# Optimization experiments

Measured on AMD Instinct MI355X. Metric: run time of the kernel, lower is better.

Reference implementation:

```python
import jax, jax.numpy as jnp
import numpy as np
from jax import lax

B, L = 128, 26          # batch, sequence length (25-iteration loop => L = 26)
C1, C2 = 128, 64        # conv channel widths (n_filters)
K1, K2 = 7, 5           # conv kernel sizes
N_POS = 25              # hardcoded position loop in original module
H = 1 + L * C2 + (C2 * C2) * (N_POS * (N_POS + 1) // 2)  # 1332865


def setup_inputs() -> dict:
    key = jax.random.key(0)
    ks = jax.random.split(key, 6)
    x = jax.random.randint(ks[0], (B, L), 0, 4)                      # nucleotide ids 0..3
    conv1_w = jax.random.normal(ks[1], (C1, 4, K1), jnp.float32) * 0.1
    conv1_b = jnp.zeros((C1,), jnp.float32)
    conv2_w = jax.random.normal(ks[2], (C2, C1, K2), jnp.float32) * 0.05
    conv2_b = jnp.zeros((C2,), jnp.float32)
    reg_w = jax.random.normal(ks[3], (1, H), jnp.float32) * 0.001
    reg_b = jnp.zeros((1,), jnp.float32)
    return {"x": x, "conv1_w": conv1_w, "conv1_b": conv1_b,
            "conv2_w": conv2_w, "conv2_b": conv2_b,
            "reg_w": reg_w, "reg_b": reg_b}


def _conv1d_same_relu(h, w, b):
    # torch Conv1d(padding=k//2) + ReLU; dropout p=0.0 is identity (eval)
    k = w.shape[-1]
    y = lax.conv_general_dilated(h, w, (1,), [(k // 2, k // 2)],
                                 dimension_numbers=('NCH', 'OIH', 'NCH'))
    return jax.nn.relu(y + b[None, :, None])


def reference(x, conv1_w, conv1_b, conv2_w, conv2_b, reg_w, reg_b):
    # one_hot(x).transpose(1,2) -> [B, 4, L]
    h = jax.nn.one_hot(x, 4, dtype=jnp.float32).transpose(0, 2, 1)
    h = _conv1d_same_relu(h, conv1_w, conv1_b)   # [B, C1, L]
    h = _conv1d_same_relu(h, conv2_w, conv2_b)   # [B, C2, L]
    # permute(0,2,1).reshape(B, -1): position-major, channel-minor flat features
    feat = h.transpose(0, 2, 1).reshape(h.shape[0], -1)  # [B, L*C2]
    # pairwise quadratic expansion: for position i, channel j -> feat[:, i*C+j] * feat[:, (i+1)*C:]
    # vectorized per-position as an outer product; 25-iteration structural loop only
    parts = []
    for i in range(N_POS):
        a = feat[:, i * C2:(i + 1) * C2]          # [B, C2]
        b = feat[:, (i + 1) * C2:]                # [B, (L-1-i)*C2]
        parts.append((a[:, :, None] * b[:, None, :]).reshape(feat.shape[0], -1))
    x_second_order = jnp.concatenate(parts, axis=1)       # [B, 325*C2^2]
    full = jnp.concatenate(
        [jnp.ones((feat.shape[0], 1), jnp.float32), feat, x_second_order], axis=1)  # [B, H]
    out = full @ reg_w[0] + reg_b[0]              # Linear(H, 1) -> squeeze -> [B]
    return out
```

## Files before the change

kernel.cpp:

```cpp
#include <hip/hip_runtime.h>

#define B_   128
#define L_   26
#define C1_  128
#define C2_  64
#define K1_  7
#define K2_  5
#define NPOS 25
#define FEAT (L_*C2_)
#define NPAIR (NPOS*(NPOS+1)/2)

#define HROW 132
#define WROW 644

__global__ __launch_bounds__(256) void conv_kernel(
    const int*   __restrict__ x,
    const float* __restrict__ w1, const float* __restrict__ b1,
    const float* __restrict__ w2, const float* __restrict__ b2,
    float* __restrict__ featT)
{
    __shared__ float h1s[30*HROW];
    __shared__ float w2s[16*WROW];
    __shared__ float w1s[4*K1_*C1_];
    __shared__ int   xs[L_];

    const int bid = blockIdx.x;
    const int b   = bid >> 2;
    const int c2t = bid & 3;
    const int t   = threadIdx.x;

    if (t < L_) xs[t] = x[b*L_ + t];
    if (t < HROW) { h1s[0*HROW+t] = 0.f; h1s[1*HROW+t] = 0.f;
                    h1s[28*HROW+t] = 0.f; h1s[29*HROW+t] = 0.f; }

    for (int i = t; i < C1_*4*K1_; i += 256) {
        const int c1  = i / (4*K1_);
        const int rem = i - c1*(4*K1_);
        const int nt  = rem / K1_;
        const int k   = rem - nt*K1_;
        w1s[(nt*K1_ + k)*C1_ + c1] = w1[i];
    }

    {
        const float* src = w2 + c2t*16*C1_*K2_;
        for (int idx = t; idx < 16*C1_*K2_; idx += 256) {
            const int c2i = idx / (C1_*K2_);
            const int rem = idx - c2i*(C1_*K2_);
            const int c1  = rem / K2_;
            const int k   = rem - c1*K2_;
            w2s[c2i*WROW + k*C1_ + c1] = src[idx];
        }
    }
    __syncthreads();

    for (int idx = t; idx < C1_*L_; idx += 256) {
        const int c1 = idx & 127;
        const int l  = idx >> 7;
        float s = b1[c1];
        #pragma unroll
        for (int k = 0; k < K1_; ++k) {
            const int pos = l + k - 3;
            if (pos >= 0 && pos < L_)
                s += w1s[(xs[pos]*K1_ + k)*C1_ + c1];
        }
        h1s[(l+2)*HROW + c1] = fmaxf(s, 0.f);
    }
    __syncthreads();

    if (t < 16*13) {
        const int c2i = t & 15;
        const int lg  = t >> 4;
        const int l0  = 2*lg, l1 = 2*lg + 1;
        float a0 = 0.f, a1 = 0.f, a2 = 0.f, a3 = 0.f;
        #pragma unroll
        for (int k = 0; k < K2_; ++k) {
            const float4* wrow = (const float4*)&w2s[c2i*WROW + k*C1_];
            const float4* h0r  = (const float4*)&h1s[(l0 + k)*HROW];
            const float4* h1r  = (const float4*)&h1s[(l1 + k)*HROW];
            #pragma unroll
            for (int cq = 0; cq < 32; cq += 2) {
                const float4 w0 = wrow[cq],  w1v = wrow[cq+1];
                const float4 x0 = h0r[cq],   x1 = h0r[cq+1];
                const float4 y0 = h1r[cq],   y1 = h1r[cq+1];
                a0 += w0.x*x0.x + w0.y*x0.y + w0.z*x0.z + w0.w*x0.w;
                a1 += w1v.x*x1.x + w1v.y*x1.y + w1v.z*x1.z + w1v.w*x1.w;
                a2 += w0.x*y0.x + w0.y*y0.y + w0.z*y0.z + w0.w*y0.w;
                a3 += w1v.x*y1.x + w1v.y*y1.y + w1v.z*y1.z + w1v.w*y1.w;
            }
        }
        const int   c2  = c2t*16 + c2i;
        const float bb  = b2[c2];
        featT[(l0*C2_ + c2)*B_ + b] = fmaxf(a0 + a1 + bb, 0.f);
        featT[(l1*C2_ + c2)*B_ + b] = fmaxf(a2 + a3 + bb, 0.f);
    }
}

__global__ __launch_bounds__(256) void reg_kernel(
    const float* __restrict__ featT,
    const float* __restrict__ rw, const float* __restrict__ rb,
    float* __restrict__ part)
{
    __shared__ float ws[64*64];
    __shared__ float red0[256], red1[256];
    const int t  = threadIdx.x;
    const int b0 = t & 63;
    const int wv = t >> 6;
    const int bid = blockIdx.x;

    float acc0 = 0.f, acc1 = 0.f;

    if (bid == NPAIR) {
        const int u0 = wv * (FEAT/4);
        for (int u = u0; u < u0 + FEAT/4; ++u) {
            const float w = rw[1 + u];
            acc0 += featT[u*B_ + b0]      * w;
            acc1 += featT[u*B_ + b0 + 64] * w;
        }
        if (wv == 0) { const float c = rw[0] + rb[0]; acc0 += c; acc1 += c; }
    } else {
        int i = 0, r = bid;
        while (r >= NPOS - i) { r -= NPOS - i; ++i; }
        const int j = i + 1 + r;

        const int stride = (NPOS - i) * 64;
        const int base   = 1 + FEAT + 4096*(NPOS*i - (i*(i-1))/2)
                         + (j - i - 1)*64;

        #pragma unroll
        for (int k = 0; k < 16; ++k) {
            const int idx = t + k*256;
            ws[idx] = rw[base + (idx >> 6)*stride + (idx & 63)];
        }
        __syncthreads();

        const int p0 = wv * 16;
        float sp0[16], sp1[16];
        #pragma unroll
        for (int pp = 0; pp < 16; ++pp) { sp0[pp] = 0.f; sp1[pp] = 0.f; }

        const float* fj = &featT[j*64*B_ + b0];
        #pragma unroll 4
        for (int g = 0; g < 16; ++g) {
            const float f00 = fj[(g*4+0)*B_],      f01 = fj[(g*4+1)*B_],
                        f02 = fj[(g*4+2)*B_],      f03 = fj[(g*4+3)*B_];
            const float f10 = fj[(g*4+0)*B_ + 64], f11 = fj[(g*4+1)*B_ + 64],
                        f12 = fj[(g*4+2)*B_ + 64], f13 = fj[(g*4+3)*B_ + 64];
            #pragma unroll
            for (int pp = 0; pp < 16; ++pp) {
                const float4 w = *(const float4*)&ws[(p0 + pp)*64 + g*4];
                sp0[pp] += w.x*f00 + w.y*f01 + w.z*f02 + w.w*f03;
                sp1[pp] += w.x*f10 + w.y*f11 + w.z*f12 + w.w*f13;
            }
        }

        const float* fi = &featT[(i*64 + p0)*B_ + b0];
        #pragma unroll
        for (int pp = 0; pp < 16; ++pp) {
            acc0 += fi[pp*B_]      * sp0[pp];
            acc1 += fi[pp*B_ + 64] * sp1[pp];
        }
    }

    red0[t] = acc0;
    red1[t] = acc1;
    __syncthreads();
    if (t < B_) {
        const int bb = t & 63;
        const float* rr = (t < 64) ? red0 : red1;
        part[bid*B_ + t] = (rr[bb] + rr[64+bb]) + (rr[128+bb] + rr[192+bb]);
    }
}

__global__ __launch_bounds__(128) void fin_kernel(
    const float* __restrict__ part, float* __restrict__ out)
{
    const int b = threadIdx.x;
    float s0 = 0.f, s1 = 0.f, s2 = 0.f, s3 = 0.f;
    int p = 0;
    for (; p + 4 <= NPAIR + 1; p += 4) {
        s0 += part[(p+0)*B_ + b];
        s1 += part[(p+1)*B_ + b];
        s2 += part[(p+2)*B_ + b];
        s3 += part[(p+3)*B_ + b];
    }
    for (; p < NPAIR + 1; ++p) s0 += part[p*B_ + b];
    out[b] = (s0 + s1) + (s2 + s3);
}

extern "C" void kernel_launch(void* const* d_in, const int* in_sizes, int n_in,
                              void* d_out, int out_size, void* d_ws, size_t ws_size,
                              hipStream_t stream)
{
    const int*   x  = (const int*)  d_in[0];
    const float* w1 = (const float*)d_in[1];
    const float* b1 = (const float*)d_in[2];
    const float* w2 = (const float*)d_in[3];
    const float* b2 = (const float*)d_in[4];
    const float* rw = (const float*)d_in[5];
    const float* rb = (const float*)d_in[6];
    float* out   = (float*)d_out;
    float* featT = (float*)d_ws;
    float* part  = (float*)((char*)d_ws + 851968);

    conv_kernel<<<dim3(512), dim3(256), 0, stream>>>(x, w1, b1, w2, b2, featT);
    reg_kernel <<<dim3(NPAIR+1), dim3(256), 0, stream>>>(featT, rw, rb, part);
    fin_kernel <<<dim3(1), dim3(128), 0, stream>>>(part, out);
}
```

Before: 115.0 us.

## Fuse final reduction into reg kernel via last-block counter; rebalance conv tiling

The separate final-sum kernel is removed. Each reg block now bumps an atomic counter after writing its partial, and the last block to arrive sums all partials into the output, which saves one kernel launch. The conv kernel now runs 256 blocks of 128 threads, each covering half the output channels. Each thread computes 4 channels × 2 positions so weight and activation loads from shared memory are reused more. The conv kernel resets the counter to zero each call, which relies on stream ordering, and conv has fewer, larger blocks that use more shared memory each.

New measurement: 141.3 us. 1.23x slower.

```diff
diff --git a/kernel.cpp b/kernel.cpp
--- a/kernel.cpp
+++ b/kernel.cpp
@@ -11,29 +11,33 @@
 #define NPAIR (NPOS*(NPOS+1)/2)
 
 #define HROW 132
-#define WROW 644
-
-__global__ __launch_bounds__(256) void conv_kernel(
+#define W2ROW 644
+
+__global__ __launch_bounds__(128) void conv_kernel(
     const int*   __restrict__ x,
     const float* __restrict__ w1, const float* __restrict__ b1,
     const float* __restrict__ w2, const float* __restrict__ b2,
-    float* __restrict__ featT)
+    float* __restrict__ featT, int* __restrict__ counter)
 {
+    __shared__ float w2s[32*W2ROW];
     __shared__ float h1s[30*HROW];
-    __shared__ float w2s[16*WROW];
     __shared__ float w1s[4*K1_*C1_];
     __shared__ int   xs[L_];
 
-    const int bid = blockIdx.x;
-    const int b   = bid >> 2;
-    const int c2t = bid & 3;
-    const int t   = threadIdx.x;
+    const int bid  = blockIdx.x;
+    const int b    = bid >> 1;
+    const int half = bid & 1;
+    const int t    = threadIdx.x;
+
+    if (bid == 0 && t == 0) *counter = 0;
 
     if (t < L_) xs[t] = x[b*L_ + t];
-    if (t < HROW) { h1s[0*HROW+t] = 0.f; h1s[1*HROW+t] = 0.f;
-                    h1s[28*HROW+t] = 0.f; h1s[29*HROW+t] = 0.f; }
-
-    for (int i = t; i < C1_*4*K1_; i += 256) {
+    for (int i = t; i < HROW; i += 128) {
+        h1s[0*HROW+i] = 0.f; h1s[1*HROW+i] = 0.f;
+        h1s[28*HROW+i] = 0.f; h1s[29*HROW+i] = 0.f;
+    }
+
+    for (int i = t; i < C1_*4*K1_; i += 128) {
         const int c1  = i / (4*K1_);
         const int rem = i - c1*(4*K1_);
         const int nt  = rem / K1_;
@@ -42,18 +46,21 @@
     }
 
     {
-        const float* src = w2 + c2t*16*C1_*K2_;
-        for (int idx = t; idx < 16*C1_*K2_; idx += 256) {
-            const int c2i = idx / (C1_*K2_);
-            const int rem = idx - c2i*(C1_*K2_);
-            const int c1  = rem / K2_;
-            const int k   = rem - c1*K2_;
-            w2s[c2i*WROW + k*C1_ + c1] = src[idx];
-        }
-    }
-    __syncthreads();
-
-    for (int idx = t; idx < C1_*L_; idx += 256) {
+        const float* src = w2 + half*32*C1_*K2_;
+        #pragma unroll
+        for (int i = 0; i < 32; ++i) {
+            const int p  = t + i*128;
+            const int c2 = p >> 7;
+            const int c1 = p & 127;
+            const float* s5 = src + p*5;
+            float* dst = &w2s[c2*W2ROW + c1];
+            dst[0*C1_] = s5[0]; dst[1*C1_] = s5[1]; dst[2*C1_] = s5[2];
+            dst[3*C1_] = s5[3]; dst[4*C1_] = s5[4];
+        }
+    }
+    __syncthreads();
+
+    for (int idx = t; idx < C1_*L_; idx += 128) {
         const int c1 = idx & 127;
         const int l  = idx >> 7;
         float s = b1[c1];
@@ -67,41 +74,63 @@
     }
     __syncthreads();
 
-    if (t < 16*13) {
-        const int c2i = t & 15;
-        const int lg  = t >> 4;
-        const int l0  = 2*lg, l1 = 2*lg + 1;
-        float a0 = 0.f, a1 = 0.f, a2 = 0.f, a3 = 0.f;
-        #pragma unroll
+    if (t < 104) {
+        const int c2t = t / 13;
+        const int lt  = t - c2t*13;
+        const int l0  = 2*lt, l1 = l0 + 1;
+
+        float acc00=0.f, acc01=0.f, acc02=0.f, acc03=0.f;
+        float acc10=0.f, acc11=0.f, acc12=0.f, acc13=0.f;
+        const float* wbase = &w2s[(c2t*4)*W2ROW];
+
         for (int k = 0; k < K2_; ++k) {
-            const float4* wrow = (const float4*)&w2s[c2i*WROW + k*C1_];
-            const float4* h0r  = (const float4*)&h1s[(l0 + k)*HROW];
-            const float4* h1r  = (const float4*)&h1s[(l1 + k)*HROW];
-            #pragma unroll
-            for (int cq = 0; cq < 32; cq += 2) {
-                const float4 w0 = wrow[cq],  w1v = wrow[cq+1];
-                const float4 x0 = h0r[cq],   x1 = h0r[cq+1];
-                const float4 y0 = h1r[cq],   y1 = h1r[cq+1];
-                a0 += w0.x*x0.x + w0.y*x0.y + w0.z*x0.z + w0.w*x0.w;
-                a1 += w1v.x*x1.x + w1v.y*x1.y + w1v.z*x1.z + w1v.w*x1.w;
-                a2 += w0.x*y0.x + w0.y*y0.y + w0.z*y0.z + w0.w*y0.w;
-                a3 += w1v.x*y1.x + w1v.y*y1.y + w1v.z*y1.z + w1v.w*y1.w;
+            const float4* hr0 = (const float4*)&h1s[(l0 + k)*HROW];
+            const float4* hr1 = (const float4*)&h1s[(l1 + k)*HROW];
+            const float*  wk  = wbase + k*C1_;
+            #pragma unroll 4
+            for (int q = 0; q < 32; ++q) {
+                const float4 h0 = hr0[q];
+                const float4 h1v = hr1[q];
+                const float4 w0 = *(const float4*)&wk[0*W2ROW + q*4];
+                const float4 w1v= *(const float4*)&wk[1*W2ROW + q*4];
+                const float4 w2v= *(const float4*)&wk[2*W2ROW + q*4];
+                const float4 w3 = *(const float4*)&wk[3*W2ROW + q*4];
+                acc00 += w0.x*h0.x + w0.y*h0.y + w0.z*h0.z + w0.w*h0.w;
+                acc01 += w1v.x*h0.x + w1v.y*h0.y + w1v.z*h0.z + w1v.w*h0.w;
+                acc02 += w2v.x*h0.x + w2v.y*h0.y + w2v.z*h0.z + w2v.w*h0.w;
+                acc03 += w3.x*h0.x + w3.y*h0.y + w3.z*h0.z + w3.w*h0.w;
+                acc10 += w0.x*h1v.x + w0.y*h1v.y + w0.z*h1v.z + w0.w*h1v.w;
+                acc11 += w1v.x*h1v.x + w1v.y*h1v.y + w1v.z*h1v.z + w1v.w*h1v.w;
+                acc12 += w2v.x*h1v.x + w2v.y*h1v.y + w2v.z*h1v.z + w2v.w*h1v.w;
+                acc13 += w3.x*h1v.x + w3.y*h1v.y + w3.z*h1v.z + w3.w*h1v.w;
             }
         }
-        const int   c2  = c2t*16 + c2i;
-        const float bb  = b2[c2];
-        featT[(l0*C2_ + c2)*B_ + b] = fmaxf(a0 + a1 + bb, 0.f);
-        featT[(l1*C2_ + c2)*B_ + b] = fmaxf(a2 + a3 + bb, 0.f);
+
+        const int c2g = half*32 + c2t*4;
+        const float bb0 = b2[c2g+0], bb1 = b2[c2g+1],
+                    bb2 = b2[c2g+2], bb3 = b2[c2g+3];
+        float* f0 = &featT[(l0*C2_ + c2g)*B_ + b];
+        float* f1 = &featT[(l1*C2_ + c2g)*B_ + b];
+        f0[0*B_] = fmaxf(acc00 + bb0, 0.f);
+        f0[1*B_] = fmaxf(acc01 + bb1, 0.f);
+        f0[2*B_] = fmaxf(acc02 + bb2, 0.f);
+        f0[3*B_] = fmaxf(acc03 + bb3, 0.f);
+        f1[0*B_] = fmaxf(acc10 + bb0, 0.f);
+        f1[1*B_] = fmaxf(acc11 + bb1, 0.f);
+        f1[2*B_] = fmaxf(acc12 + bb2, 0.f);
+        f1[3*B_] = fmaxf(acc13 + bb3, 0.f);
     }
 }
 
 __global__ __launch_bounds__(256) void reg_kernel(
     const float* __restrict__ featT,
     const float* __restrict__ rw, const float* __restrict__ rb,
-    float* __restrict__ part)
+    float* __restrict__ part, int* __restrict__ counter,
+    float* __restrict__ out)
 {
     __shared__ float ws[64*64];
     __shared__ float red0[256], red1[256];
+    __shared__ int   isLast;
     const int t  = threadIdx.x;
     const int b0 = t & 63;
     const int wv = t >> 6;
@@ -169,22 +198,26 @@
         const float* rr = (t < 64) ? red0 : red1;
         part[bid*B_ + t] = (rr[bb] + rr[64+bb]) + (rr[128+bb] + rr[192+bb]);
     }
-}
-
-__global__ __launch_bounds__(128) void fin_kernel(
-    const float* __restrict__ part, float* __restrict__ out)
-{
-    const int b = threadIdx.x;
-    float s0 = 0.f, s1 = 0.f, s2 = 0.f, s3 = 0.f;
-    int p = 0;
-    for (; p + 4 <= NPAIR + 1; p += 4) {
-        s0 += part[(p+0)*B_ + b];
-        s1 += part[(p+1)*B_ + b];
-        s2 += part[(p+2)*B_ + b];
-        s3 += part[(p+3)*B_ + b];
-    }
-    for (; p < NPAIR + 1; ++p) s0 += part[p*B_ + b];
-    out[b] = (s0 + s1) + (s2 + s3);
+
+    __threadfence();
+    __syncthreads();
+    if (t == 0) isLast = (atomicAdd(counter, 1) == NPAIR);
+    __syncthreads();
+    if (isLast) {
+        __threadfence();
+        if (t < B_) {
+            float s0 = 0.f, s1 = 0.f, s2 = 0.f, s3 = 0.f;
+            int p = 0;
+            for (; p + 4 <= NPAIR + 1; p += 4) {
+                s0 += part[(p+0)*B_ + t];
+                s1 += part[(p+1)*B_ + t];
+                s2 += part[(p+2)*B_ + t];
+                s3 += part[(p+3)*B_ + t];
+            }
+            for (; p < NPAIR + 1; ++p) s0 += part[p*B_ + t];
+            out[t] = (s0 + s1) + (s2 + s3);
+        }
+    }
 }
 
 extern "C" void kernel_launch(void* const* d_in, const int* in_sizes, int n_in,
@@ -198,11 +231,13 @@
     const float* b2 = (const float*)d_in[4];
     const float* rw = (const float*)d_in[5];
     const float* rb = (const float*)d_in[6];
-    float* out   = (float*)d_out;
-    float* featT = (float*)d_ws;
-    float* part  = (float*)((char*)d_ws + 851968);
-
-    conv_kernel<<<dim3(512), dim3(256), 0, stream>>>(x, w1, b1, w2, b2, featT);
-    reg_kernel <<<dim3(NPAIR+1), dim3(256), 0, stream>>>(featT, rw, rb, part);
-    fin_kernel <<<dim3(1), dim3(128), 0, stream>>>(part, out);
+    float* out     = (float*)d_out;
+    float* featT   = (float*)d_ws;
+    float* part    = (float*)((char*)d_ws + 851968);
+    int*   counter = (int*)  ((char*)d_ws + 851968 + 166912);
+
+    conv_kernel<<<dim3(256), dim3(128), 0, stream>>>(x, w1, b1, w2, b2,
+                                                     featT, counter);
+    reg_kernel <<<dim3(NPAIR+1), dim3(256), 0, stream>>>(featT, rw, rb,
+                                                         part, counter, out);
 }
```

## Split conv stage into separate conv1 and conv2 kernels with batch-minor layout

Applied to the files above, without the earlier changes.

The fused per-sample conv kernel is replaced by two kernels. The first computes conv1 with threads mapped to batch and writes a zero-padded, batch-minor h1 buffer to global memory. The second computes conv2 per (position, 8-channel group), splitting the C1 reduction across four waves and combining the partial sums in shared memory. This is meant to cut the redundant per-block reloading of w2 and the low thread utilisation of the old kernel, at the cost of an extra launch and a global round-trip for h1.

Result: slower. 126.9 us (+10.3%).

```diff
diff --git a/kernel.cpp b/kernel.cpp
--- a/kernel.cpp
+++ b/kernel.cpp
@@ -9,89 +9,121 @@
 #define NPOS 25
 #define FEAT (L_*C2_)
 #define NPAIR (NPOS*(NPOS+1)/2)
-
-#define HROW 132
-#define WROW 644
-
-__global__ __launch_bounds__(256) void conv_kernel(
+#define HR   30
+
+
+__global__ __launch_bounds__(128) void s_kernel(
     const int*   __restrict__ x,
     const float* __restrict__ w1, const float* __restrict__ b1,
-    const float* __restrict__ w2, const float* __restrict__ b2,
-    float* __restrict__ featT)
-{
-    __shared__ float h1s[30*HROW];
-    __shared__ float w2s[16*WROW];
-    __shared__ float w1s[4*K1_*C1_];
-    __shared__ int   xs[L_];
-
+    float* __restrict__ h1g)
+{
     const int bid = blockIdx.x;
-    const int b   = bid >> 2;
-    const int c2t = bid & 3;
     const int t   = threadIdx.x;
 
-    if (t < L_) xs[t] = x[b*L_ + t];
-    if (t < HROW) { h1s[0*HROW+t] = 0.f; h1s[1*HROW+t] = 0.f;
-                    h1s[28*HROW+t] = 0.f; h1s[29*HROW+t] = 0.f; }
-
-    for (int i = t; i < C1_*4*K1_; i += 256) {
-        const int c1  = i / (4*K1_);
-        const int rem = i - c1*(4*K1_);
-        const int nt  = rem / K1_;
-        const int k   = rem - nt*K1_;
-        w1s[(nt*K1_ + k)*C1_ + c1] = w1[i];
-    }
-
-    {
-        const float* src = w2 + c2t*16*C1_*K2_;
-        for (int idx = t; idx < 16*C1_*K2_; idx += 256) {
-            const int c2i = idx / (C1_*K2_);
-            const int rem = idx - c2i*(C1_*K2_);
-            const int c1  = rem / K2_;
-            const int k   = rem - c1*K2_;
-            w2s[c2i*WROW + k*C1_ + c1] = src[idx];
-        }
-    }
-    __syncthreads();
-
-    for (int idx = t; idx < C1_*L_; idx += 256) {
-        const int c1 = idx & 127;
-        const int l  = idx >> 7;
-        float s = b1[c1];
+    if (bid >= 104) {
+        const int z   = bid - 104;
+        const int c1q = z >> 2;
+        const int pr  = z & 3;
+        const int row = (pr < 2) ? pr : 26 + pr;
+        #pragma unroll
+        for (int ci = 0; ci < 32; ++ci)
+            h1g[((c1q*32 + ci)*HR + row)*B_ + t] = 0.f;
+        return;
+    }
+
+    const int l   = bid % 26;
+    const int c1q = bid / 26;
+
+    __shared__ float w1s[4*K1_*32];
+    for (int i = t; i < 4*K1_*32; i += 128) {
+        const int ci  = i / (4*K1_);
+        const int rem = i - ci*(4*K1_);
+        w1s[rem*32 + ci] = w1[(c1q*32 + ci)*(4*K1_) + rem];
+    }
+    __syncthreads();
+
+    int xv[K1_];
+    #pragma unroll
+    for (int k = 0; k < K1_; ++k) {
+        const int pos = l + k - 3;
+        xv[k] = (pos >= 0 && pos < L_) ? x[t*L_ + pos] : 0;
+    }
+
+    for (int ci = 0; ci < 32; ++ci) {
+        float s = b1[c1q*32 + ci];
         #pragma unroll
         for (int k = 0; k < K1_; ++k) {
             const int pos = l + k - 3;
             if (pos >= 0 && pos < L_)
-                s += w1s[(xs[pos]*K1_ + k)*C1_ + c1];
-        }
-        h1s[(l+2)*HROW + c1] = fmaxf(s, 0.f);
-    }
-    __syncthreads();
-
-    if (t < 16*13) {
-        const int c2i = t & 15;
-        const int lg  = t >> 4;
-        const int l0  = 2*lg, l1 = 2*lg + 1;
-        float a0 = 0.f, a1 = 0.f, a2 = 0.f, a3 = 0.f;
+                s += w1s[(xv[k]*K1_ + k)*32 + ci];
+        }
+        h1g[((c1q*32 + ci)*HR + (l + 2))*B_ + t] = fmaxf(s, 0.f);
+    }
+}
+
+__global__ __launch_bounds__(256) void g_kernel(
+    const float* __restrict__ h1g,
+    const float* __restrict__ w2, const float* __restrict__ b2,
+    float* __restrict__ featT)
+{
+    __shared__ float w2s[K2_*C1_*8];
+    __shared__ float red[4*8*B_];
+
+    const int bid = blockIdx.x;
+    const int l   = bid % 26;
+    const int c2o = bid / 26;
+    const int t   = threadIdx.x;
+    const int wv  = t >> 6;
+    const int b0  = t & 63;
+
+    for (int idx = t; idx < K2_*C1_*8; idx += 256) {
+        const int c2i = idx / (C1_*K2_);
+        const int rem = idx - c2i*(C1_*K2_);
+        const int c1  = rem / K2_;
+        const int k   = rem - c1*K2_;
+        w2s[(k*C1_ + c1)*8 + c2i] = w2[(c2o*8 + c2i)*(C1_*K2_) + rem];
+    }
+    __syncthreads();
+
+    float acc[8][2];
+    #pragma unroll
+    for (int c = 0; c < 8; ++c) { acc[c][0] = 0.f; acc[c][1] = 0.f; }
+
+    const int cb = wv*32;
+    for (int c1i = 0; c1i < 32; ++c1i) {
+        const int c1 = cb + c1i;
+        const float* hbase = &h1g[(c1*HR + l)*B_];
         #pragma unroll
         for (int k = 0; k < K2_; ++k) {
-            const float4* wrow = (const float4*)&w2s[c2i*WROW + k*C1_];
-            const float4* h0r  = (const float4*)&h1s[(l0 + k)*HROW];
-            const float4* h1r  = (const float4*)&h1s[(l1 + k)*HROW];
-            #pragma unroll
-            for (int cq = 0; cq < 32; cq += 2) {
-                const float4 w0 = wrow[cq],  w1v = wrow[cq+1];
-                const float4 x0 = h0r[cq],   x1 = h0r[cq+1];
-                const float4 y0 = h1r[cq],   y1 = h1r[cq+1];
-                a0 += w0.x*x0.x + w0.y*x0.y + w0.z*x0.z + w0.w*x0.w;
-                a1 += w1v.x*x1.x + w1v.y*x1.y + w1v.z*x1.z + w1v.w*x1.w;
-                a2 += w0.x*y0.x + w0.y*y0.y + w0.z*y0.z + w0.w*y0.w;
-                a3 += w1v.x*y1.x + w1v.y*y1.y + w1v.z*y1.z + w1v.w*y1.w;
-            }
-        }
-        const int   c2  = c2t*16 + c2i;
-        const float bb  = b2[c2];
-        featT[(l0*C2_ + c2)*B_ + b] = fmaxf(a0 + a1 + bb, 0.f);
-        featT[(l1*C2_ + c2)*B_ + b] = fmaxf(a2 + a3 + bb, 0.f);
+            const float h0 = hbase[k*B_ + b0];
+            const float h1 = hbase[k*B_ + b0 + 64];
+            const float4* wp = (const float4*)&w2s[(k*C1_ + c1)*8];
+            const float4 wa = wp[0], wb = wp[1];
+            acc[0][0] += wa.x*h0;  acc[0][1] += wa.x*h1;
+            acc[1][0] += wa.y*h0;  acc[1][1] += wa.y*h1;
+            acc[2][0] += wa.z*h0;  acc[2][1] += wa.z*h1;
+            acc[3][0] += wa.w*h0;  acc[3][1] += wa.w*h1;
+            acc[4][0] += wb.x*h0;  acc[4][1] += wb.x*h1;
+            acc[5][0] += wb.y*h0;  acc[5][1] += wb.y*h1;
+            acc[6][0] += wb.z*h0;  acc[6][1] += wb.z*h1;
+            acc[7][0] += wb.w*h0;  acc[7][1] += wb.w*h1;
+        }
+    }
+
+    #pragma unroll
+    for (int c = 0; c < 8; ++c) {
+        red[(wv*8 + c)*B_ + b0]      = acc[c][0];
+        red[(wv*8 + c)*B_ + b0 + 64] = acc[c][1];
+    }
+    __syncthreads();
+
+    for (int u = t; u < 8*B_; u += 256) {
+        const int c2i = u >> 7;
+        const int bb  = u & 127;
+        float s = red[(0*8 + c2i)*B_ + bb] + red[(1*8 + c2i)*B_ + bb]
+                + red[(2*8 + c2i)*B_ + bb] + red[(3*8 + c2i)*B_ + bb];
+        s += b2[c2o*8 + c2i];
+        featT[(l*C2_ + c2o*8 + c2i)*B_ + bb] = fmaxf(s, 0.f);
     }
 }
 
@@ -199,10 +231,12 @@
     const float* rw = (const float*)d_in[5];
     const float* rb = (const float*)d_in[6];
     float* out   = (float*)d_out;
-    float* featT = (float*)d_ws;
-    float* part  = (float*)((char*)d_ws + 851968);
-
-    conv_kernel<<<dim3(512), dim3(256), 0, stream>>>(x, w1, b1, w2, b2, featT);
-    reg_kernel <<<dim3(NPAIR+1), dim3(256), 0, stream>>>(featT, rw, rb, part);
-    fin_kernel <<<dim3(1), dim3(128), 0, stream>>>(part, out);
-}
+    float* h1g   = (float*)d_ws;
+    float* featT = (float*)((char*)d_ws + 1966080);
+    float* part  = (float*)((char*)d_ws + 2818048);
+
+    s_kernel  <<<dim3(120), dim3(128), 0, stream>>>(x, w1, b1, h1g);
+    g_kernel  <<<dim3(208), dim3(256), 0, stream>>>(h1g, w2, b2, featT);
+    reg_kernel<<<dim3(NPAIR+1), dim3(256), 0, stream>>>(featT, rw, rb, part);
+    fin_kernel<<<dim3(1), dim3(128), 0, stream>>>(part, out);
+}
```
